# Kernel optimization log

Measured on AMD Instinct MI355X. Metric: run time of the kernel, lower is better.

The kernel has to match this reference:

```python
import jax, jax.numpy as jnp
import numpy as np

B, N, D, HID, S, NH = 2, 384, 768, 256, 64, 8


def layernorm(x, g, b, eps=1e-5):
    m = x.mean(-1, keepdims=True)
    v = ((x - m) ** 2).mean(-1, keepdims=True)
    return (x - m) * jax.lax.rsqrt(v + eps) * g + b


def setup_inputs() -> dict:
    key = jax.random.key(0)
    ks = jax.random.split(key, 32)
    r = lambda i, shp: jax.random.normal(ks[i], shp, dtype=jnp.float32) * 0.02
    inp = {
        'coordinates': jax.random.normal(ks[0], (B, N, 3), dtype=jnp.float32),
        'features': jax.random.normal(ks[1], (B, N, D), dtype=jnp.float32),
        'superpoint_labels': jax.random.randint(ks[2], (B, N), 0, S),
        # geometric_encoder: Linear(9,HID)-LN-ReLU-Linear(HID,D)-LN
        'ge_w1': r(3, (9, HID)), 'ge_b1': jnp.zeros((HID,)),
        'ge_g1': jnp.ones((HID,)), 'ge_be1': jnp.zeros((HID,)),
        'ge_w2': r(4, (HID, D)), 'ge_b2': jnp.zeros((D,)),
        'ge_g2': jnp.ones((D,)), 'ge_be2': jnp.zeros((D,)),
        # superpoint_aggregator: Linear(D,HID)-LN-ReLU-Linear(HID,D)-LN
        'ag_w1': r(5, (D, HID)), 'ag_b1': jnp.zeros((HID,)),
        'ag_g1': jnp.ones((HID,)), 'ag_be1': jnp.zeros((HID,)),
        'ag_w2': r(6, (HID, D)), 'ag_b2': jnp.zeros((D,)),
        'ag_g2': jnp.ones((D,)), 'ag_be2': jnp.zeros((D,)),
        # spatial_attention (MultiheadAttention, 8 heads)
        'wq': r(7, (D, D)), 'bq': jnp.zeros((D,)),
        'wk': r(8, (D, D)), 'bk': jnp.zeros((D,)),
        'wv': r(9, (D, D)), 'bv': jnp.zeros((D,)),
        'wo': r(10, (D, D)), 'bo': jnp.zeros((D,)),
    }
    return inp


def _forward(coordinates, features, superpoint_labels,
             ge_w1, ge_b1, ge_g1, ge_be1, ge_w2, ge_b2, ge_g2, ge_be2,
             ag_w1, ag_b1, ag_g1, ag_be1, ag_w2, ag_b2, ag_g2, ag_be2,
             wq, bq, wk, bk, wv, bv, wo, bo):
    # pairwise geometric relations: [B,N,N,9]
    rp = coordinates[:, :, None, :] - coordinates[:, None, :, :]
    dist = jnp.linalg.norm(rp, axis=-1, keepdims=True)
    rn = rp / jnp.maximum(dist, 1e-12)  # F.normalize semantics
    z = jnp.zeros_like(rn[..., 0])
    # torch loop writes channels (i*3+j-3): (0,1)->-2==3, (0,2)->-1==4, (1,2)->2; ch 0,1 stay zero
    ang = jnp.stack([z, z, rn[..., 1] * rn[..., 2],
                     rn[..., 0] * rn[..., 1], rn[..., 0] * rn[..., 2]], axis=-1)
    rel = jnp.concatenate([dist, rn, ang], axis=-1)
    h = jax.nn.relu(layernorm(rel @ ge_w1 + ge_b1, ge_g1, ge_be1))
    enc = layernorm(h @ ge_w2 + ge_b2, ge_g2, ge_be2)  # [B,N,N,D]
    geo_ctx = enc.mean(axis=2)  # [B,N,D]
    # per-superpoint scatter-mean (vectorized over all groups)
    oh = jax.nn.one_hot(superpoint_labels, S, dtype=features.dtype)  # [B,N,S]
    cnt = oh.sum(axis=1)  # [B,S]
    denom = jnp.maximum(cnt, 1.0)[..., None]
    mean_f = jnp.einsum('bns,bnd->bsd', oh, features) / denom
    mean_g = jnp.einsum('bns,bnd->bsd', oh, geo_ctx) / denom
    ah = jax.nn.relu(layernorm(mean_f @ ag_w1 + ag_b1, ag_g1, ag_be1))
    agg = layernorm(ah @ ag_w2 + ag_b2, ag_g2, ag_be2)
    combined = agg + mean_g  # [B,S,D]
    bidx = jnp.arange(B)[:, None]
    comb_g = combined[bidx, superpoint_labels]  # gather back [B,N,D]
    valid = (cnt[bidx, superpoint_labels] >= 2.0)[..., None]
    cw = 0.3  # consistency_weight
    enhanced = jnp.where(valid, (1.0 - cw) * features + cw * comb_g, features)
    # cross-attention: q=enhanced, k=v=geo_ctx
    dh = D // NH
    q = (enhanced @ wq + bq).reshape(B, N, NH, dh).transpose(0, 2, 1, 3)
    k = (geo_ctx @ wk + bk).reshape(B, N, NH, dh).transpose(0, 2, 1, 3)
    v = (geo_ctx @ wv + bv).reshape(B, N, NH, dh).transpose(0, 2, 1, 3)
    attn = jax.nn.softmax(jnp.einsum('bhqd,bhkd->bhqk', q, k) * (dh ** -0.5), axis=-1)
    o = jnp.einsum('bhqk,bhkd->bhqd', attn, v).transpose(0, 2, 1, 3).reshape(B, N, D)
    spatial = o @ wo + bo
    return enhanced + 0.5 * spatial


def reference(coordinates, features, superpoint_labels,
              ge_w1, ge_b1, ge_g1, ge_be1, ge_w2, ge_b2, ge_g2, ge_be2,
              ag_w1, ag_b1, ag_g1, ag_be1, ag_w2, ag_b2, ag_g2, ag_be2,
              wq, bq, wk, bk, wv, bv, wo, bo):
    return _forward(coordinates, features, superpoint_labels,
                    ge_w1, ge_b1, ge_g1, ge_be1, ge_w2, ge_b2, ge_g2, ge_be2,
                    ag_w1, ag_b1, ag_g1, ag_be1, ag_w2, ag_b2, ag_g2, ag_be2,
                    wq, bq, wk, bk, wv, bv, wo, bo)
```

## Files before the change

kernel.cpp:

```cpp
#include <hip/hip_runtime.h>
#include <hip/hip_bf16.h>
#include <stdint.h>
#include <stddef.h>

#define BB 2
#define NN 384
#define DD 768
#define HH 256
#define SS 64
#define NHH 8
#define DHH 96

typedef __attribute__((ext_vector_type(8))) short bf16x8;
typedef __attribute__((ext_vector_type(4))) float f32x4;

__device__ __forceinline__ float bits_f(unsigned short u){
  unsigned x = ((unsigned)u) << 16; float f; __builtin_memcpy(&f, &x, 4); return f;
}
__device__ __forceinline__ unsigned short f_bits(float a){
  unsigned x; __builtin_memcpy(&x, &a, 4);
  unsigned r = x + 0x7fffu + ((x >> 16) & 1u);
  return (unsigned short)(r >> 16);
}
__device__ __forceinline__ float lo_f(unsigned u){ unsigned x = u << 16; float f; __builtin_memcpy(&f,&x,4); return f; }
// ... 113 lines not shown
    f32x4 acc = (f32x4){0.f,0.f,0.f,0.f};
    for (int ks = 0; ks < 24; ++ks){
      bf16x8 af = *(const bf16x8*)&w2r[(size_t)(ti*16 + l16)*768 + ks*32 + quad*8];
      bf16x8 bf = *(const bf16x8*)&w2r[(size_t)(tj*16 + l16)*768 + ks*32 + quad*8];
      acc = __builtin_amdgcn_mfma_f32_16x16x32_bf16(af, bf, acc, 0,0,0);
    }
    #pragma unroll
    for (int r = 0; r < 4; ++r)
      Gm[(ti*16 + quad*4 + r)*256 + tj*16 + l16] = (short)f_bits(acc[r]);
  } else if (blk == 64){
    for (int c = tid; c < 768; c += 256) b2s[c] = b2[c];
    __syncthreads();
    float sa = 0.f, wa = 0.f;
    const uint4* wr = (const uint4*)(w2r + (size_t)tid*768);
    #pragma unroll 4
    for (int kk = 0; kk < 96; ++kk){
      uint4 ww = wr[kk];
      const float* bp = &b2s[kk*8];
      float x0=lo_f(ww.x), x1=hi_f(ww.x), x2=lo_f(ww.y), x3=hi_f(ww.y);
      float x4=lo_f(ww.z), x5=hi_f(ww.z), x6=lo_f(ww.w), x7=hi_f(ww.w);
      sa += (x0+x1)+(x2+x3)+(x4+x5)+(x6+x7);
      wa += bp[0]*x0 + bp[1]*x1 + bp[2]*x2 + bp[3]*x3
          + bp[4]*x4 + bp[5]*x5 + bp[6]*x6 + bp[7]*x7;
    }
    Gm[256*256 + tid] = (short)f_bits(sa);
    Gm[257*256 + tid] = (short)f_bits(wa);
    #pragma unroll
    for (int rr = 258; rr < 288; ++rr) Gm[rr*256 + tid] = 0;
    float pb = 0.f, pbb = 0.f;
    for (int c = tid; c < 768; c += 256){ float bb = b2s[c]; pb += bb; pbb += bb*bb; }
    for (int m = 32; m >= 1; m >>= 1){ pb += __shfl_xor(pb,m); pbb += __shfl_xor(pbb,m); }
    if ((tid & 63) == 0){ red[tid>>6] = pb; red[4+(tid>>6)] = pbb; }
    __syncthreads();
    if (tid == 0){ gscal[0] = red[0]+red[1]+red[2]+red[3]; gscal[1] = red[4]+red[5]+red[6]+red[7]; }
  } else {
    const unsigned short* w1u = (const unsigned short*)w1t;
    if (tid < 81){
      int i = tid / 9, j = tid % 9;
      float acc = 0.f;
      for (int c = 0; c < 256; ++c)
        acc += bits_f(w1u[c*32 + i]) * bits_f(w1u[c*32 + j]);
      g1s[18 + tid] = acc;
    } else if (tid < 90){
      int i = tid - 81;
      float sa = 0.f, sb = 0.f;
      for (int c = 0; c < 256; ++c){
        float x = bits_f(w1u[c*32 + i]);
        sa += x; sb += x * b1[c];
      }
      g1s[i] = sa; g1s[9 + i] = sb;
    } else if (tid == 90){
      float pb = 0.f, pbb = 0.f;
      for (int c = 0; c < 256; ++c){ float bb = b1[c]; pb += bb; pbb += bb*bb; }
      g1s[99] = pb; g1s[100] = pbb;
    }
  }
}

__global__ __launch_bounds__(256, 3) void k_geo(
    const float* __restrict__ coord, const short* __restrict__ w1t,
    const float* __restrict__ b1g, const float* __restrict__ g1g, const float* __restrict__ be1g,
    const short* __restrict__ Gm, const float* __restrict__ gscal,
    const float* __restrict__ g1s, float* __restrict__ gv)
{
  __shared__ short relbf[64*36];
  __shared__ short h_bf[64*256];
  __shared__ float rmean[64], rrstd[64];
  __shared__ float msum[64], wbsum[64], qsum[64];

  const int tid = threadIdx.x;
  const int pair = blockIdx.x % 768;
  const int jt   = blockIdx.x / 768;
  const int j0 = jt * 64;
  const int b = pair / NN;

  if (tid < 64){
    int j = j0 + tid;
    float cix = coord[pair*3+0], ciy = coord[pair*3+1], ciz = coord[pair*3+2];
    float dx = cix - coord[(b*NN+j)*3+0];
    float dy = ciy - coord[(b*NN+j)*3+1];
    float dz = ciz - coord[(b*NN+j)*3+2];
    float dist = sqrtf(dx*dx + dy*dy + dz*dz);
    float inv = 1.f / fmaxf(dist, 1e-12f);
    float x = dx*inv, y = dy*inv, z = dz*inv;
    float rv[9];
    rv[0]=dist; rv[1]=x; rv[2]=y; rv[3]=z; rv[4]=0.f; rv[5]=0.f;
    rv[6]=y*z; rv[7]=x*y; rv[8]=x*z;
    short* rr = &relbf[tid*36];
    float rbf[9];
    #pragma unroll
    for (int k=0;k<9;++k){
      unsigned short hb = f_bits(rv[k]);
      rr[k] = (short)hb; rbf[k] = bits_f(hb);
    }
    #pragma unroll
    for (int k=9;k<32;++k) rr[k]=0;
    float s = g1s[99], ssq = g1s[100];
    #pragma unroll
    for (int i=0;i<9;++i){
      s += rbf[i]*g1s[i];
      ssq += 2.f*rbf[i]*g1s[9+i];
      #pragma unroll
      for (int jj=0;jj<9;++jj) ssq += rbf[i]*rbf[jj]*g1s[18+i*9+jj];
    }
    float mean = s*(1.f/256.f);
    float var  = ssq*(1.f/256.f) - mean*mean;
    rmean[tid] = mean; rrstd[tid] = rsqrtf(var + 1e-5f);
  } else if (tid < 128){
    qsum[tid-64] = 0.f;
  }
  __syncthreads();

  const int wave = tid >> 6, lane = tid & 63, quad = lane >> 4, l16 = lane & 15;

  unsigned hreg[4][4][2];
  {
    bf16x8 af[4];
    #pragma unroll
    for (int rb=0;rb<4;++rb)
      af[rb] = *(const bf16x8*)&relbf[(rb*16 + l16)*36 + quad*8];
    f32x4 hacc[4][4];
    #pragma unroll
    for (int ci=0;ci<4;++ci){
      int cb = wave*4 + ci;
      bf16x8 bfw = *(const bf16x8*)&w1t[(cb*16 + l16)*32 + quad*8];
      #pragma unroll
      for (int rb=0;rb<4;++rb)
        hacc[ci][rb] = __builtin_amdgcn_mfma_f32_16x16x32_bf16(af[rb], bfw, (f32x4){0.f,0.f,0.f,0.f}, 0,0,0);
    }
    f32x4 rmv[4], rsv[4];
    #pragma unroll
    for (int rb=0;rb<4;++rb){
      rmv[rb] = *(const f32x4*)&rmean[rb*16 + quad*4];
      rsv[rb] = *(const f32x4*)&rrstd[rb*16 + quad*4];
    }
    #pragma unroll
    for (int ci=0;ci<4;++ci){
      int col = (wave*4+ci)*16 + l16;
      float b1c = b1g[col], g1c = g1g[col], be1c = be1g[col];
      int chb = col >> 3, lo = col & 7;
      #pragma unroll
      for (int rb=0;rb<4;++rb){
        float hn[4];
        #pragma unroll
        for (int r=0;r<4;++r)
          hn[r] = fmaxf((hacc[ci][rb][r] + b1c - rmv[rb][r]) * rsv[rb][r] * g1c + be1c, 0.f);
        unsigned p0 = cvt_pk_bf16(hn[0], hn[1]);
        unsigned p1 = cvt_pk_bf16(hn[2], hn[3]);
        hreg[ci][rb][0] = p0; hreg[ci][rb][1] = p1;
        int row0 = rb*16 + quad*4;
        h_bf[(row0+0)*256 + ((chb + row0+0)&31)*8 + lo] = (short)(p0 & 0xffff);
        h_bf[(row0+1)*256 + ((chb + row0+1)&31)*8 + lo] = (short)(p0 >> 16);
        h_bf[(row0+2)*256 + ((chb + row0+2)&31)*8 + lo] = (short)(p1 & 0xffff);
        h_bf[(row0+3)*256 + ((chb + row0+3)&31)*8 + lo] = (short)(p1 >> 16);
      }
    }
  }
  __syncthreads();

  {
    f32x4 acc[4][4];
    #pragma unroll
    for (int ci=0;ci<4;++ci)
      #pragma unroll
      for (int rb=0;rb<4;++rb) acc[ci][rb] = (f32x4){0.f,0.f,0.f,0.f};
    f32x4 eacc[4];
    #pragma unroll
    for (int rb=0;rb<4;++rb) eacc[rb] = (f32x4){0.f,0.f,0.f,0.f};
    for (int ks=0;ks<8;++ks){
      bf16x8 a4[4];
      #pragma unroll
      for (int rb=0;rb<4;++rb){
        int row = rb*16 + l16;
        a4[rb] = *(const bf16x8*)&h_bf[row*256 + (((ks*4 + quad) + row)&31)*8];
      }
      #pragma unroll
      for (int ci=0;ci<4;++ci){
        int n = (wave*4+ci)*16 + l16;
        bf16x8 bg = *(const bf16x8*)&Gm[n*256 + ks*32 + quad*8];
        #pragma unroll
        for (int rb=0;rb<4;++rb)
          acc[ci][rb] = __builtin_amdgcn_mfma_f32_16x16x32_bf16(a4[rb], bg, acc[ci][rb], 0,0,0);
      }
      if (wave == 0){
        bf16x8 bge = *(const bf16x8*)&Gm[(256 + l16)*256 + ks*32 + quad*8];
        #pragma unroll
        for (int rb=0;rb<4;++rb)
          eacc[rb] = __builtin_amdgcn_mfma_f32_16x16x32_bf16(a4[rb], bge, eacc[rb], 0,0,0);
      }
    }
    if (wave == 0 && l16 < 2){
      float* dst = (l16 == 0) ? msum : wbsum;
      #pragma unroll
      for (int rb=0;rb<4;++rb)
        #pragma unroll
        for (int r=0;r<4;++r) dst[rb*16 + quad*4 + r] = eacc[rb][r];
    }
    #pragma unroll
    for (int rb=0;rb<4;++rb){
      #pragma unroll
      for (int r=0;r<4;++r){
        int row = rb*16 + quad*4 + r;
        float qp = 0.f;
        #pragma unroll
        for (int ci=0;ci<4;++ci){
          unsigned p = hreg[ci][rb][r>>1];
          float hv = (r & 1) ? hi_f(p) : lo_f(p);
          qp += acc[ci][rb][r] * hv;
        }
        qp += __shfl_xor(qp,1);
        qp += __shfl_xor(qp,2);
        qp += __shfl_xor(qp,4);
        qp += __shfl_xor(qp,8);
        if (l16 == 0) atomicAdd(&qsum[row], qp);
      }
    }
  }
  __syncthreads();
  if (tid < 64){
    float Sb = gscal[0], Sbb = gscal[1];
    float m2 = (msum[tid] + Sb)*(1.f/768.f);
    float ssq = qsum[tid] + 2.f*wbsum[tid] + Sbb;
    float var = ssq*(1.f/768.f) - m2*m2;
    rmean[tid] = m2; rrstd[tid] = rsqrtf(var + 1e-5f);
  }
  __syncthreads();
  float* gp = gv + ((size_t)pair*6 + jt)*258;
  if (tid < 64){
    float rr = rrstd[tid], tt = rmean[tid]*rrstd[tid];
    for (int m = 32; m >= 1; m >>= 1){ rr += __shfl_xor(rr,m); tt += __shfl_xor(tt,m); }
    if (tid == 0){ gp[256] = rr; gp[257] = tt; }
  }
  {
    float vp[4] = {0.f, 0.f, 0.f, 0.f};
    #pragma unroll
    for (int rb=0;rb<4;++rb){
      #pragma unroll
      for (int r=0;r<4;++r){
        int row = rb*16 + quad*4 + r;
        float rs = rrstd[row];
        #pragma unroll
        for (int ci=0;ci<4;++ci){
          unsigned p = hreg[ci][rb][r>>1];
          float hv = (r & 1) ? hi_f(p) : lo_f(p);
          vp[ci] += rs * hv;
        }
      }
    }
    #pragma unroll
    for (int ci=0;ci<4;++ci){
      vp[ci] += __shfl_xor(vp[ci],16);
      vp[ci] += __shfl_xor(vp[ci],32);
    }
    if (quad == 0){
      #pragma unroll
      for (int ci=0;ci<4;++ci)
        gp[(wave*4+ci)*16 + l16] = vp[ci];
    }
  }
}

__global__ __launch_bounds__(256) void k_geofin(
    const float* __restrict__ gv, const short* __restrict__ w2r,
    const float* __restrict__ b2g, const float* __restrict__ g2g,
    const float* __restrict__ be2g, unsigned short* __restrict__ geo)
{
  __shared__ float V[256];
  __shared__ float RT[2];
  const int tid = threadIdx.x, pair = blockIdx.x;
  const float* gp = gv + (size_t)pair*6*258;
  V[tid] = gp[tid] + gp[258 + tid] + gp[2*258 + tid]
         + gp[3*258 + tid] + gp[4*258 + tid] + gp[5*258 + tid];
  if (tid < 2){
    float r = 0.f;
    #pragma unroll
    for (int t = 0; t < 6; ++t) r += gp[t*258 + 256 + tid];
    RT[tid] = r;
  }
  __syncthreads();
  const float R = RT[0], T = RT[1];
  const unsigned short* wr = (const unsigned short*)w2r;
  float a0 = 0.f, a1 = 0.f, a2 = 0.f;
  #pragma unroll 4
  for (int k = 0; k < 256; ++k){
    float vk = V[k];
    const unsigned short* row = wr + (size_t)k*768;
    a0 += vk * bits_f(row[tid]);
    a1 += vk * bits_f(row[tid+256]);
    a2 += vk * bits_f(row[tid+512]);
  }
  size_t base = (size_t)pair*DD;
  geo[base + tid]       = f_bits(g2g[tid]    *(a0 + b2g[tid]    *R - T)*(1.f/384.f) + be2g[tid]);
  geo[base + tid + 256] = f_bits(g2g[tid+256]*(a1 + b2g[tid+256]*R - T)*(1.f/384.f) + be2g[tid+256]);
  geo[base + tid + 512] = f_bits(g2g[tid+512]*(a2 + b2g[tid+512]*R - T)*(1.f/384.f) + be2g[tid+512]);
}

__global__ __launch_bounds__(256) void k_agg(
    const int* __restrict__ lab, const float* __restrict__ feat,
    const unsigned short* __restrict__ geo, float* __restrict__ cntw,
    const short* __restrict__ w1T, const float* __restrict__ b1g,
    const float* __restrict__ g1g, const float* __restrict__ be1g,
    const short* __restrict__ w2T, const float* __restrict__ b2g,
    const float* __restrict__ g2g, const float* __restrict__ be2g,
    float* __restrict__ comb)
{
  __shared__ int ls[NN];
  __shared__ float xr[DD];
  __shared__ float hr[HH];
  __shared__ float red[8];
  const int tid = threadIdx.x;
  const int bs = blockIdx.x, b = bs >> 6, s = bs & 63;
  for (int j = tid; j < NN; j += 256) ls[j] = lab[b*NN + j];
  __syncthreads();
  float f0 = 0.f, f1 = 0.f, f2 = 0.f, gg0 = 0.f, gg1 = 0.f, gg2 = 0.f;
  int cnt = 0;
  for (int j = 0; j < NN; ++j){
    if (ls[j] == s){
      ++cnt;
      size_t rb = (size_t)(b*NN + j)*DD;
      f0  += feat[rb + tid];
      f1  += feat[rb + tid + 256];
      f2  += feat[rb + tid + 512];
      gg0 += bits_f(geo[rb + tid]);
      gg1 += bits_f(geo[rb + tid + 256]);
      gg2 += bits_f(geo[rb + tid + 512]);
    }
  }
  const float inv = 1.f / fmaxf((float)cnt, 1.f);
  if (tid == 0) cntw[bs] = (float)cnt;
  xr[tid]       = f0*inv;
  xr[tid + 256] = f1*inv;
  xr[tid + 512] = f2*inv;
  float gmean[3] = { gg0*inv, gg1*inv, gg2*inv };
  __syncthreads();
  float a = b1g[tid];
  {
    const uint4* wr = (const uint4*)(w1T + (size_t)tid*768);
    #pragma unroll 4
    for (int kk = 0; kk < 96; ++kk){
      uint4 ww = wr[kk];
      const float* xp = &xr[kk*8];
      a += xp[0]*lo_f(ww.x) + xp[1]*hi_f(ww.x)
         + xp[2]*lo_f(ww.y) + xp[3]*hi_f(ww.y)
         + xp[4]*lo_f(ww.z) + xp[5]*hi_f(ww.z)
         + xp[6]*lo_f(ww.w) + xp[7]*hi_f(ww.w);
    }
  }
  float sum1 = a, q1 = a*a;
  for (int m = 32; m >= 1; m >>= 1){ sum1 += __shfl_xor(sum1,m); q1 += __shfl_xor(q1,m); }
  if ((tid & 63) == 0){ red[tid>>6] = sum1; red[4+(tid>>6)] = q1; }
  __syncthreads();
  sum1 = red[0]+red[1]+red[2]+red[3]; q1 = red[4]+red[5]+red[6]+red[7];
  float mean = sum1*(1.f/HH), var = q1*(1.f/HH) - mean*mean, rstd = rsqrtf(var + 1e-5f);
  float h = fmaxf((a-mean)*rstd*g1g[tid] + be1g[tid], 0.f);
  hr[tid] = h;
  __syncthreads();
  float y[3];
  #pragma unroll
  for (int u = 0; u < 3; ++u){
    int c = tid + 256*u;
    float t = b2g[c];
    const uint4* wr = (const uint4*)(w2T + (size_t)c*256);
    #pragma unroll 4
    for (int kk = 0; kk < 32; ++kk){
      uint4 ww = wr[kk];
      const float* hp = &hr[kk*8];
      t += hp[0]*lo_f(ww.x) + hp[1]*hi_f(ww.x)
         + hp[2]*lo_f(ww.y) + hp[3]*hi_f(ww.y)
         + hp[4]*lo_f(ww.z) + hp[5]*hi_f(ww.z)
         + hp[6]*lo_f(ww.w) + hp[7]*hi_f(ww.w);
    }
    y[u] = t;
  }
  float s2 = y[0]+y[1]+y[2], q2 = y[0]*y[0]+y[1]*y[1]+y[2]*y[2];
  for (int m = 32; m >= 1; m >>= 1){ s2 += __shfl_xor(s2,m); q2 += __shfl_xor(q2,m); }
  __syncthreads();
  if ((tid & 63) == 0){ red[tid>>6] = s2; red[4+(tid>>6)] = q2; }
  __syncthreads();
  s2 = red[0]+red[1]+red[2]+red[3]; q2 = red[4]+red[5]+red[6]+red[7];
  float mean2 = s2*(1.f/DD), rstd2 = rsqrtf(q2*(1.f/DD) - mean2*mean2 + 1e-5f);
  size_t base = (size_t)bs * DD;
  #pragma unroll
  for (int u = 0; u < 3; ++u){
    int c = tid + 256*u;
    comb[base + c] = (y[u]-mean2)*rstd2*g2g[c] + be2g[c] + gmean[u];
  }
}

__global__ void k_enhance(const float* __restrict__ feat, const int* __restrict__ lab,
                          const float* __restrict__ cntw, const float* __restrict__ comb,
                          float* __restrict__ enh, unsigned short* __restrict__ enhb)
{
  int idx = blockIdx.x * 256 + threadIdx.x;
  int c = idx % DD; int bn = idx / DD; int b = bn / NN;
  int l = lab[bn];
  float f = feat[idx];
  float cg = comb[(size_t)(b*SS + l)*DD + c];
  float cnt = cntw[b*SS + l];
  float e = (cnt >= 2.0f) ? (0.7f*f + 0.3f*cg) : f;
  enh[idx] = e;
  enhb[idx] = f_bits(e);
}

__global__ __launch_bounds__(256, 4) void k_qkv(
    const unsigned short* __restrict__ enhb, const unsigned short* __restrict__ geo,
    const short* __restrict__ wqT, const short* __restrict__ wkT, const short* __restrict__ wvT,
    const float* __restrict__ bq, const float* __restrict__ bk, const float* __restrict__ bv,
    unsigned short* __restrict__ qo, unsigned short* __restrict__ ko, unsigned short* __restrict__ vo)
{
  const int tid = threadIdx.x, blk = blockIdx.x;
  const int m = blk / 144, rem = blk % 144;
  const int rt = rem / 3, ct = rem % 3;
  const int wave = tid >> 6, lane = tid & 63, quad = lane >> 4, l16 = lane & 15;
  const short* WT = (m==0)?wqT:(m==1)?wkT:wvT;
  const float* Bv = (m==0)?bq:(m==1)?bk:bv;
  unsigned short* Y = (m==0)?qo:(m==1)?ko:vo;
  const short* X = (const short*)((m==0)? enhb : geo);
  const float oscale = (m==0)? 0.10206207261596577f : 1.0f;
  const int row0 = rt*16;
  const int col0 = ct*256 + wave*64;

  f32x4 acc[4];
  #pragma unroll
  for (int cb=0;cb<4;++cb) acc[cb] = (f32x4){0.f,0.f,0.f,0.f};
  for (int ks = 0; ks < 24; ++ks){
    bf16x8 af = *(const bf16x8*)&X[(size_t)(row0 + l16)*DD + ks*32 + quad*8];
    #pragma unroll
    for (int cb=0;cb<4;++cb){
      bf16x8 bw = *(const bf16x8*)&WT[(size_t)(col0 + cb*16 + l16)*DD + ks*32 + quad*8];
      acc[cb] = __builtin_amdgcn_mfma_f32_16x16x32_bf16(af, bw, acc[cb], 0,0,0);
    }
  }
  #pragma unroll
  for (int cb=0;cb<4;++cb){
    int col = col0 + cb*16 + l16;
    float bb = Bv[col];
    #pragma unroll
    for (int r=0;r<4;++r){
      int row = row0 + quad*4 + r;
      Y[(size_t)row*DD + col] = f_bits((acc[cb][r] + bb)*oscale);
    }
  }
}

__global__ __launch_bounds__(256) void k_attn_split(
    const unsigned short* __restrict__ qws, const unsigned short* __restrict__ kws,
    const unsigned short* __restrict__ vws, float* __restrict__ pws)
{
  __shared__ short kt[64*104];
  __shared__ short vt[64*104];
  __shared__ float st[32*66];
  __shared__ float lsum[32];
  const int tid = threadIdx.x;
  const int half = blockIdx.x / 192;
  const int inner = blockIdx.x % 192;
  const int b = inner / (NHH*12); int rem = inner % (NHH*12);
  const int h = rem / 12; const int qt = rem % 12; const int q0 = qt*32;
  const int sq = tid >> 3, jp = tid & 7;
  const int qp = tid >> 4, dp = tid & 15;
  unsigned qreg[48];
  {
    const unsigned* qr = (const unsigned*)(qws + (size_t)(b*NN + q0 + sq)*DD + h*DHH);
    #pragma unroll
    for (int d2 = 0; d2 < 48; ++d2) qreg[d2] = qr[d2];
  }
  if (tid < 32) lsum[tid] = 0.f;
  float Oacc[2][6];
  #pragma unroll
  for (int a = 0; a < 2; ++a)
    #pragma unroll
    for (int m = 0; m < 6; ++m) Oacc[a][m] = 0.f;

  for (int jt = half*3; jt < half*3 + 3; ++jt){
    const int j0 = jt * 64;
    __syncthreads();
    for (int x = tid; x < 64*48; x += 256){
      int jl = x / 48, du = x % 48;
      size_t rowoff = (size_t)(b*NN + j0 + jl)*DD + h*DHH;
      ((unsigned*)&kt[jl*104])[du] = ((const unsigned*)(kws + rowoff))[du];
      ((unsigned*)&vt[jl*104])[du] = ((const unsigned*)(vws + rowoff))[du];
    }
    __syncthreads();
    float lpart = 0.f;
    #pragma unroll
    for (int jj = 0; jj < 8; ++jj){
      int j = jp*8 + jj;
      const uint4* kr4 = (const uint4*)&kt[j*104];
      float s = 0.f;
      #pragma unroll
      for (int d4 = 0; d4 < 12; ++d4){
        uint4 kk = kr4[d4];
        unsigned q0r = qreg[4*d4], q1r = qreg[4*d4+1], q2r = qreg[4*d4+2], q3r = qreg[4*d4+3];
        s += lo_f(kk.x)*lo_f(q0r) + hi_f(kk.x)*hi_f(q0r);
        s += lo_f(kk.y)*lo_f(q1r) + hi_f(kk.y)*hi_f(q1r);
        s += lo_f(kk.z)*lo_f(q2r) + hi_f(kk.z)*hi_f(q2r);
        s += lo_f(kk.w)*lo_f(q3r) + hi_f(kk.w)*hi_f(q3r);
      }
      float p = __expf(s);
      st[sq*66 + j] = p;
      lpart += p;
    }
    lpart += __shfl_xor(lpart,1);
    lpart += __shfl_xor(lpart,2);
    lpart += __shfl_xor(lpart,4);
    if (jp == 0) lsum[sq] += lpart;
    __syncthreads();
    #pragma unroll 4
    for (int j = 0; j < 64; ++j){
      float p0 = st[(2*qp)*66 + j];
      float p1 = st[(2*qp+1)*66 + j];
      const unsigned* vr = (const unsigned*)&vt[j*104 + dp*6];
      #pragma unroll
      for (int m = 0; m < 3; ++m){
        unsigned vv = vr[m];
        float v0 = lo_f(vv), v1 = hi_f(vv);
        Oacc[0][2*m]   += p0*v0; Oacc[0][2*m+1] += p0*v1;
        Oacc[1][2*m]   += p1*v0; Oacc[1][2*m+1] += p1*v1;
      }
    }
  }
  __syncthreads();
  float* pb = pws + ((size_t)inner*2 + half)*3104;
  #pragma unroll
  for (int m = 0; m < 6; ++m){
    pb[(2*qp)*96 + dp*6 + m]   = Oacc[0][m];
    pb[(2*qp+1)*96 + dp*6 + m] = Oacc[1][m];
  }
  if (tid < 32) pb[3072 + tid] = lsum[tid];
}

__global__ __launch_bounds__(256) void k_attnfin(
    const float* __restrict__ pws, unsigned short* __restrict__ ows)
{
  __shared__ float ls[32];
  const int tid = threadIdx.x, inner = blockIdx.x;
  const int b = inner / (NHH*12); int rem = inner % (NHH*12);
  const int h = rem / 12; const int qt = rem % 12; const int q0 = qt*32;
  const float* p0 = pws + (size_t)inner*2*3104;
  const float* p1 = p0 + 3104;
  if (tid < 32) ls[tid] = 1.f / (p0[3072+tid] + p1[3072+tid]);
  __syncthreads();
  #pragma unroll
  for (int u = 0; u < 12; ++u){
    int e = tid + u*256;
    int q = e / 96, d = e % 96;
    float o = (p0[e] + p1[e]) * ls[q];
    ows[(size_t)(b*NN + q0 + q)*DD + h*DHH + d] = f_bits(o);
  }
}

__global__ __launch_bounds__(256) void k_attn_full(
    const unsigned short* __restrict__ qws, const unsigned short* __restrict__ kws,
    const unsigned short* __restrict__ vws, unsigned short* __restrict__ ows)
{
  __shared__ short kt[64*104];
  __shared__ short vt[64*104];
  __shared__ float st[32*66];
  __shared__ float lsum[32];
  const int tid = threadIdx.x;
  const int blk = blockIdx.x;
  const int b = blk / (NHH*12); int rem = blk % (NHH*12);
  const int h = rem / 12; const int qt = rem % 12; const int q0 = qt*32;
  const int sq = tid >> 3, jp = tid & 7;
  const int qp = tid >> 4, dp = tid & 15;
  unsigned qreg[48];
  {
    const unsigned* qr = (const unsigned*)(qws + (size_t)(b*NN + q0 + sq)*DD + h*DHH);
    #pragma unroll
    for (int d2 = 0; d2 < 48; ++d2) qreg[d2] = qr[d2];
  }
  if (tid < 32) lsum[tid] = 0.f;
  float Oacc[2][6];
  #pragma unroll
  for (int a = 0; a < 2; ++a)
    #pragma unroll
    for (int m = 0; m < 6; ++m) Oacc[a][m] = 0.f;
  for (int jt = 0; jt < 6; ++jt){
    const int j0 = jt * 64;
    __syncthreads();
    for (int x = tid; x < 64*48; x += 256){
      int jl = x / 48, du = x % 48;
      size_t rowoff = (size_t)(b*NN + j0 + jl)*DD + h*DHH;
      ((unsigned*)&kt[jl*104])[du] = ((const unsigned*)(kws + rowoff))[du];
      ((unsigned*)&vt[jl*104])[du] = ((const unsigned*)(vws + rowoff))[du];
    }
    __syncthreads();
    float lpart = 0.f;
    #pragma unroll
    for (int jj = 0; jj < 8; ++jj){
      int j = jp*8 + jj;
      const uint4* kr4 = (const uint4*)&kt[j*104];
      float s = 0.f;
      #pragma unroll
      for (int d4 = 0; d4 < 12; ++d4){
        uint4 kk = kr4[d4];
        unsigned q0r = qreg[4*d4], q1r = qreg[4*d4+1], q2r = qreg[4*d4+2], q3r = qreg[4*d4+3];
        s += lo_f(kk.x)*lo_f(q0r) + hi_f(kk.x)*hi_f(q0r);
        s += lo_f(kk.y)*lo_f(q1r) + hi_f(kk.y)*hi_f(q1r);
        s += lo_f(kk.z)*lo_f(q2r) + hi_f(kk.z)*hi_f(q2r);
        s += lo_f(kk.w)*lo_f(q3r) + hi_f(kk.w)*hi_f(q3r);
      }
      float p = __expf(s);
      st[sq*66 + j] = p;
      lpart += p;
    }
    lpart += __shfl_xor(lpart,1);
    lpart += __shfl_xor(lpart,2);
    lpart += __shfl_xor(lpart,4);
    if (jp == 0) lsum[sq] += lpart;
    __syncthreads();
    #pragma unroll 4
    for (int j = 0; j < 64; ++j){
      float p0 = st[(2*qp)*66 + j];
      float p1 = st[(2*qp+1)*66 + j];
      const unsigned* vr = (const unsigned*)&vt[j*104 + dp*6];
      #pragma unroll
      for (int m = 0; m < 3; ++m){
        unsigned vv = vr[m];
        float v0 = lo_f(vv), v1 = hi_f(vv);
        Oacc[0][2*m]   += p0*v0; Oacc[0][2*m+1] += p0*v1;
        Oacc[1][2*m]   += p1*v0; Oacc[1][2*m+1] += p1*v1;
      }
    }
  }
  __syncthreads();
  float l0 = 1.f / lsum[2*qp], l1 = 1.f / lsum[2*qp+1];
  size_t ob = (size_t)(b*NN + q0)*DD + h*DHH + dp*6;
  #pragma unroll
  for (int m = 0; m < 6; ++m){
    ows[ob + (size_t)(2*qp)*DD + m]   = f_bits(Oacc[0][m]*l0);
    ows[ob + (size_t)(2*qp+1)*DD + m] = f_bits(Oacc[1][m]*l1);
  }
}

__global__ __launch_bounds__(256, 4) void k_out(
    const unsigned short* __restrict__ ows, const float* __restrict__ enh,
    const short* __restrict__ woT, const float* __restrict__ bo, float* __restrict__ out)
{
  const int tid = threadIdx.x, blk = blockIdx.x;
  const int rt = blk / 3, ct = blk % 3;
  const int wave = tid >> 6, lane = tid & 63, quad = lane >> 4, l16 = lane & 15;
  const int row0 = rt*16;
  const int col0 = ct*256 + wave*64;
  f32x4 acc[4];
  #pragma unroll
  for (int cb=0;cb<4;++cb) acc[cb] = (f32x4){0.f,0.f,0.f,0.f};
  for (int ks = 0; ks < 24; ++ks){
    bf16x8 af = *(const bf16x8*)&((const short*)ows)[(size_t)(row0 + l16)*DD + ks*32 + quad*8];
    #pragma unroll
    for (int cb=0;cb<4;++cb){
      bf16x8 bw = *(const bf16x8*)&woT[(size_t)(col0 + cb*16 + l16)*DD + ks*32 + quad*8];
      acc[cb] = __builtin_amdgcn_mfma_f32_16x16x32_bf16(af, bw, acc[cb], 0,0,0);
    }
  }
  #pragma unroll
  for (int cb=0;cb<4;++cb){
    int col = col0 + cb*16 + l16;
    float bb = bo[col];
    #pragma unroll
    for (int r=0;r<4;++r){
      size_t idx = (size_t)(row0 + quad*4 + r)*DD + col;
      out[idx] = enh[idx] + 0.5f*(acc[cb][r] + bb);
    }
  }
}

extern "C" void kernel_launch(void* const* d_in, const int* in_sizes, int n_in,
                              void* d_out, int out_size, void* d_ws, size_t ws_size,
                              hipStream_t stream) {
  const float* coord = (const float*)d_in[0];
  const float* feat  = (const float*)d_in[1];
  const int*   lab   = (const int*)d_in[2];
  const float* ge_w1 = (const float*)d_in[3];
  const float* ge_b1 = (const float*)d_in[4];
  const float* ge_g1 = (const float*)d_in[5];
  const float* ge_be1= (const float*)d_in[6];
  const float* ge_w2 = (const float*)d_in[7];
  const float* ge_b2 = (const float*)d_in[8];
  const float* ge_g2 = (const float*)d_in[9];
  const float* ge_be2= (const float*)d_in[10];
  const float* ag_w1 = (const float*)d_in[11];
  const float* ag_b1 = (const float*)d_in[12];
  const float* ag_g1 = (const float*)d_in[13];
  const float* ag_be1= (const float*)d_in[14];
  const float* ag_w2 = (const float*)d_in[15];
  const float* ag_b2 = (const float*)d_in[16];
  const float* ag_g2 = (const float*)d_in[17];
  const float* ag_be2= (const float*)d_in[18];
  const float* wq = (const float*)d_in[19];
  const float* bq = (const float*)d_in[20];
  const float* wk = (const float*)d_in[21];
  const float* bk = (const float*)d_in[22];
  const float* wv = (const float*)d_in[23];
  const float* bv = (const float*)d_in[24];
  const float* wo = (const float*)d_in[25];
  const float* bo = (const float*)d_in[26];

  char* w = (char*)d_ws;
  unsigned short* geo_bf = (unsigned short*)(w);
  float*          enh_f  = (float*)(w + 1179648);
  unsigned short* enh_bf = (unsigned short*)(w + 3538944);
  unsigned short* qw_bf  = (unsigned short*)(w + 4718592);
  unsigned short* kw_bf  = (unsigned short*)(w + 5898240);
  unsigned short* vw_bf  = (unsigned short*)(w + 7077888);
  float*          gv     = (float*)(w + 4718592);
  float*          cntw   = (float*)(w + 9842688);
  float*          comb   = (float*)(w + 9843200);
  short*          w2T    = (short*)(w + 10236416);
  short*          w2r    = (short*)(w + 10629632);
  short*          w1t    = (short*)(w + 11022848);
  short*          Gm     = (short*)(w + 11039232);
  float*          g1s    = (float*)(w + 11186688);
  float*          gscal  = (float*)(w + 11187200);
  short*          wqT    = (short*)(w + 11187456);
  short*          wkT    = (short*)(w + 12367104);
  short*          wvT    = (short*)(w + 13546752);
  short*          woT    = (short*)(w + 14726400);
  short*          agw1T  = (short*)(w + 15906048);
  short*          agw2T  = (short*)(w + 16299264);
  float*          pws    = (float*)(w + 16692480);
  unsigned short* ow_bf  = geo_bf;
  const bool split_attn = (ws_size >= 21460224);

  hipLaunchKernelGGL(k_prep,    dim3(1520),  dim3(256), 0, stream,
                     ge_w2, ge_w1, wq, wk, wv, wo, ag_w1, ag_w2,
                     w2T, w2r, wqT, wkT, wvT, woT, w1t, agw1T, agw2T);
  hipLaunchKernelGGL(k_gprep,   dim3(66),    dim3(256), 0, stream,
                     w2r, ge_b2, w1t, ge_b1, Gm, gscal, g1s);
  hipLaunchKernelGGL(k_geo,     dim3(4608),  dim3(256), 0, stream,
                     coord, w1t, ge_b1, ge_g1, ge_be1, Gm, gscal, g1s, gv);
  hipLaunchKernelGGL(k_geofin,  dim3(768),   dim3(256), 0, stream,
                     gv, w2r, ge_b2, ge_g2, ge_be2, geo_bf);
  hipLaunchKernelGGL(k_agg,     dim3(128),   dim3(256), 0, stream,
                     lab, feat, geo_bf, cntw, agw1T, ag_b1, ag_g1, ag_be1,
                     agw2T, ag_b2, ag_g2, ag_be2, comb);
  hipLaunchKernelGGL(k_enhance, dim3(2304),  dim3(256), 0, stream,
                     feat, lab, cntw, comb, enh_f, enh_bf);
  hipLaunchKernelGGL(k_qkv,     dim3(432),   dim3(256), 0, stream,
                     enh_bf, geo_bf, wqT, wkT, wvT, bq, bk, bv, qw_bf, kw_bf, vw_bf);
  if (split_attn){
    hipLaunchKernelGGL(k_attn_split, dim3(384), dim3(256), 0, stream,
                       qw_bf, kw_bf, vw_bf, pws);
    hipLaunchKernelGGL(k_attnfin,    dim3(192), dim3(256), 0, stream,
                       pws, ow_bf);
  } else {
    hipLaunchKernelGGL(k_attn_full,  dim3(192), dim3(256), 0, stream,
                       qw_bf, kw_bf, vw_bf, ow_bf);
  }
  hipLaunchKernelGGL(k_out,     dim3(144),   dim3(256), 0, stream,
                     ow_bf, enh_f, woT, bo, (float*)d_out);
}
```

Measured before the change: 426.6 us.

## Fuse enhance into QKV/out GEMMs and attention finalize into output projection

Removes the standalone enhance kernel by recomputing the consistency blend on the fly inside the Q projection's A-operand load and the output epilogue. It also drops the split-attention finalize kernel: the output projection reads both fp32 partials and the row sums directly, normalising and converting them to bf16 as it loads. This saves two launches and the enh/ows intermediate round-trips. In exchange it reads fp32 data, twice the bytes of the bf16 tiles it replaces, inside the GEMM inner loops, and repeats the blend for each column tile.

```diff
diff --git a/kernel.cpp b/kernel.cpp
--- a/kernel.cpp
+++ b/kernel.cpp
@@ -524,23 +524,10 @@
   }
 }
 
-__global__ void k_enhance(const float* __restrict__ feat, const int* __restrict__ lab,
-                          const float* __restrict__ cntw, const float* __restrict__ comb,
-                          float* __restrict__ enh, unsigned short* __restrict__ enhb)
-{
-  int idx = blockIdx.x * 256 + threadIdx.x;
-  int c = idx % DD; int bn = idx / DD; int b = bn / NN;
-  int l = lab[bn];
-  float f = feat[idx];
-  float cg = comb[(size_t)(b*SS + l)*DD + c];
-  float cnt = cntw[b*SS + l];
-  float e = (cnt >= 2.0f) ? (0.7f*f + 0.3f*cg) : f;
-  enh[idx] = e;
-  enhb[idx] = f_bits(e);
-}
-
 __global__ __launch_bounds__(256, 4) void k_qkv(
-    const unsigned short* __restrict__ enhb, const unsigned short* __restrict__ geo,
+    const float* __restrict__ feat, const int* __restrict__ lab,
+    const float* __restrict__ cntw, const float* __restrict__ comb,
+    const unsigned short* __restrict__ geo,
     const short* __restrict__ wqT, const short* __restrict__ wkT, const short* __restrict__ wvT,
     const float* __restrict__ bq, const float* __restrict__ bk, const float* __restrict__ bv,
     unsigned short* __restrict__ qo, unsigned short* __restrict__ ko, unsigned short* __restrict__ vo)
@@ -552,16 +539,48 @@
   const short* WT = (m==0)?wqT:(m==1)?wkT:wvT;
   const float* Bv = (m==0)?bq:(m==1)?bk:bv;
   unsigned short* Y = (m==0)?qo:(m==1)?ko:vo;
-  const short* X = (const short*)((m==0)? enhb : geo);
+  const short* X = (const short*)geo;
   const float oscale = (m==0)? 0.10206207261596577f : 1.0f;
   const int row0 = rt*16;
   const int col0 = ct*256 + wave*64;
 
+  const int arow = row0 + l16;
+  const float* fr = nullptr; const float* cr = nullptr; bool valid = false;
+  if (m == 0){
+    int ab = arow / NN; int l = lab[arow];
+    valid = (cntw[ab*SS + l] >= 2.0f);
+    fr = feat + (size_t)arow*DD;
+    cr = comb + (size_t)(ab*SS + l)*DD;
+  }
+
   f32x4 acc[4];
   #pragma unroll
   for (int cb=0;cb<4;++cb) acc[cb] = (f32x4){0.f,0.f,0.f,0.f};
   for (int ks = 0; ks < 24; ++ks){
-    bf16x8 af = *(const bf16x8*)&X[(size_t)(row0 + l16)*DD + ks*32 + quad*8];
+    bf16x8 af;
+    if (m == 0){
+      int c0 = ks*32 + quad*8;
+      float4 f0 = *(const float4*)&fr[c0];
+      float4 f1 = *(const float4*)&fr[c0+4];
+      float4 g0 = *(const float4*)&cr[c0];
+      float4 g1 = *(const float4*)&cr[c0+4];
+      float e0 = valid ? (0.7f*f0.x + 0.3f*g0.x) : f0.x;
+      float e1 = valid ? (0.7f*f0.y + 0.3f*g0.y) : f0.y;
+      float e2 = valid ? (0.7f*f0.z + 0.3f*g0.z) : f0.z;
+      float e3 = valid ? (0.7f*f0.w + 0.3f*g0.w) : f0.w;
+      float e4 = valid ? (0.7f*f1.x + 0.3f*g1.x) : f1.x;
+      float e5 = valid ? (0.7f*f1.y + 0.3f*g1.y) : f1.y;
+      float e6 = valid ? (0.7f*f1.z + 0.3f*g1.z) : f1.z;
+      float e7 = valid ? (0.7f*f1.w + 0.3f*g1.w) : f1.w;
+      union { unsigned u[4]; bf16x8 v; } au;
+      au.u[0] = cvt_pk_bf16(e0, e1);
+      au.u[1] = cvt_pk_bf16(e2, e3);
+      au.u[2] = cvt_pk_bf16(e4, e5);
+      au.u[3] = cvt_pk_bf16(e6, e7);
+      af = au.v;
+    } else {
+      af = *(const bf16x8*)&X[(size_t)arow*DD + ks*32 + quad*8];
+    }
     #pragma unroll
     for (int cb=0;cb<4;++cb){
       bf16x8 bw = *(const bf16x8*)&WT[(size_t)(col0 + cb*16 + l16)*DD + ks*32 + quad*8];
@@ -666,26 +685,6 @@
   if (tid < 32) pb[3072 + tid] = lsum[tid];
 }
 
-__global__ __launch_bounds__(256) void k_attnfin(
-    const float* __restrict__ pws, unsigned short* __restrict__ ows)
-{
-  __shared__ float ls[32];
-  const int tid = threadIdx.x, inner = blockIdx.x;
-  const int b = inner / (NHH*12); int rem = inner % (NHH*12);
-  const int h = rem / 12; const int qt = rem % 12; const int q0 = qt*32;
-  const float* p0 = pws + (size_t)inner*2*3104;
-  const float* p1 = p0 + 3104;
-  if (tid < 32) ls[tid] = 1.f / (p0[3072+tid] + p1[3072+tid]);
-  __syncthreads();
-  #pragma unroll
-  for (int u = 0; u < 12; ++u){
-    int e = tid + u*256;
-    int q = e / 96, d = e % 96;
-    float o = (p0[e] + p1[e]) * ls[q];
-    ows[(size_t)(b*NN + q0 + q)*DD + h*DHH + d] = f_bits(o);
-  }
-}
-
 __global__ __launch_bounds__(256) void k_attn_full(
     const unsigned short* __restrict__ qws, const unsigned short* __restrict__ kws,
     const unsigned short* __restrict__ vws, unsigned short* __restrict__ ows)
@@ -770,8 +769,81 @@
   }
 }
 
-__global__ __launch_bounds__(256, 4) void k_out(
-    const unsigned short* __restrict__ ows, const float* __restrict__ enh,
+__global__ __launch_bounds__(256, 4) void k_out_pws(
+    const float* __restrict__ pws, const float* __restrict__ feat,
+    const int* __restrict__ lab, const float* __restrict__ cntw,
+    const float* __restrict__ comb,
+    const short* __restrict__ woT, const float* __restrict__ bo, float* __restrict__ out)
+{
+  const int tid = threadIdx.x, blk = blockIdx.x;
+  const int rt = blk / 3, ct = blk % 3;
+  const int wave = tid >> 6, lane = tid & 63, quad = lane >> 4, l16 = lane & 15;
+  const int row0 = rt*16;
+  const int col0 = ct*256 + wave*64;
+
+  const int arow = row0 + l16;
+  const int ab = arow / NN, an = arow % NN;
+  const int aqt = an >> 5, aql = an & 31;
+  float lsv[8];
+  #pragma unroll
+  for (int h = 0; h < 8; ++h){
+    const float* q0p = pws + ((size_t)(ab*96 + h*12 + aqt)*2)*3104 + 3072 + aql;
+    lsv[h] = 1.f/(q0p[0] + q0p[3104]);
+  }
+
+  f32x4 acc[4];
+  #pragma unroll
+  for (int cb=0;cb<4;++cb) acc[cb] = (f32x4){0.f,0.f,0.f,0.f};
+  for (int ks = 0; ks < 24; ++ks){
+    int c0 = ks*32 + quad*8;
+    int h = c0 / 96, d0 = c0 % 96;
+    const float* pp0 = pws + ((size_t)(ab*96 + h*12 + aqt)*2)*3104 + (size_t)aql*96 + d0;
+    const float* pp1 = pp0 + 3104;
+    float4 x0 = *(const float4*)&pp0[0];
+    float4 x1 = *(const float4*)&pp0[4];
+    float4 y0 = *(const float4*)&pp1[0];
+    float4 y1 = *(const float4*)&pp1[4];
+    float ls = lsv[h];
+    union { unsigned u[4]; bf16x8 v; } au;
+    au.u[0] = cvt_pk_bf16((x0.x+y0.x)*ls, (x0.y+y0.y)*ls);
+    au.u[1] = cvt_pk_bf16((x0.z+y0.z)*ls, (x0.w+y0.w)*ls);
+    au.u[2] = cvt_pk_bf16((x1.x+y1.x)*ls, (x1.y+y1.y)*ls);
+    au.u[3] = cvt_pk_bf16((x1.z+y1.z)*ls, (x1.w+y1.w)*ls);
+    bf16x8 af = au.v;
+    #pragma unroll
+    for (int cb=0;cb<4;++cb){
+      bf16x8 bw = *(const bf16x8*)&woT[(size_t)(col0 + cb*16 + l16)*DD + ks*32 + quad*8];
+      acc[cb] = __builtin_amdgcn_mfma_f32_16x16x32_bf16(af, bw, acc[cb], 0,0,0);
+    }
+  }
+  const float* frv[4]; const float* crv[4]; bool vav[4];
+  #pragma unroll
+  for (int r=0;r<4;++r){
+    int row = row0 + quad*4 + r;
+    int bb_ = row / NN; int l = lab[row];
+    vav[r] = (cntw[bb_*SS + l] >= 2.0f);
+    frv[r] = feat + (size_t)row*DD;
+    crv[r] = comb + (size_t)(bb_*SS + l)*DD;
+  }
+  #pragma unroll
+  for (int cb=0;cb<4;++cb){
+    int col = col0 + cb*16 + l16;
+    float bb = bo[col];
+    #pragma unroll
+    for (int r=0;r<4;++r){
+      int row = row0 + quad*4 + r;
+      float f = frv[r][col];
+      float cg = crv[r][col];
+      float e = vav[r] ? (0.7f*f + 0.3f*cg) : f;
+      out[(size_t)row*DD + col] = e + 0.5f*(acc[cb][r] + bb);
+    }
+  }
+}
+
+__global__ __launch_bounds__(256, 4) void k_out_bf(
+    const unsigned short* __restrict__ ows, const float* __restrict__ feat,
+    const int* __restrict__ lab, const float* __restrict__ cntw,
+    const float* __restrict__ comb,
     const short* __restrict__ woT, const float* __restrict__ bo, float* __restrict__ out)
 {
   const int tid = threadIdx.x, blk = blockIdx.x;
@@ -790,14 +862,26 @@
       acc[cb] = __builtin_amdgcn_mfma_f32_16x16x32_bf16(af, bw, acc[cb], 0,0,0);
     }
   }
+  const float* frv[4]; const float* crv[4]; bool vav[4];
+  #pragma unroll
+  for (int r=0;r<4;++r){
+    int row = row0 + quad*4 + r;
+    int bb_ = row / NN; int l = lab[row];
+    vav[r] = (cntw[bb_*SS + l] >= 2.0f);
+    frv[r] = feat + (size_t)row*DD;
+    crv[r] = comb + (size_t)(bb_*SS + l)*DD;
+  }
   #pragma unroll
   for (int cb=0;cb<4;++cb){
     int col = col0 + cb*16 + l16;
     float bb = bo[col];
     #pragma unroll
     for (int r=0;r<4;++r){
-      size_t idx = (size_t)(row0 + quad*4 + r)*DD + col;
-      out[idx] = enh[idx] + 0.5f*(acc[cb][r] + bb);
+      int row = row0 + quad*4 + r;
+      float f = frv[r][col];
+      float cg = crv[r][col];
+      float e = vav[r] ? (0.7f*f + 0.3f*cg) : f;
+      out[(size_t)row*DD + col] = e + 0.5f*(acc[cb][r] + bb);
     }
   }
 }
@@ -835,8 +919,6 @@
 
   char* w = (char*)d_ws;
   unsigned short* geo_bf = (unsigned short*)(w);
-  float*          enh_f  = (float*)(w + 1179648);
-  unsigned short* enh_bf = (unsigned short*)(w + 3538944);
   unsigned short* qw_bf  = (unsigned short*)(w + 4718592);
   unsigned short* kw_bf  = (unsigned short*)(w + 5898240);
   unsigned short* vw_bf  = (unsigned short*)(w + 7077888);
@@ -871,19 +953,18 @@
   hipLaunchKernelGGL(k_agg,     dim3(128),   dim3(256), 0, stream,
                      lab, feat, geo_bf, cntw, agw1T, ag_b1, ag_g1, ag_be1,
                      agw2T, ag_b2, ag_g2, ag_be2, comb);
-  hipLaunchKernelGGL(k_enhance, dim3(2304),  dim3(256), 0, stream,
-                     feat, lab, cntw, comb, enh_f, enh_bf);
   hipLaunchKernelGGL(k_qkv,     dim3(432),   dim3(256), 0, stream,
-                     enh_bf, geo_bf, wqT, wkT, wvT, bq, bk, bv, qw_bf, kw_bf, vw_bf);
+                     feat, lab, cntw, comb, geo_bf, wqT, wkT, wvT,
+                     bq, bk, bv, qw_bf, kw_bf, vw_bf);
   if (split_attn){
     hipLaunchKernelGGL(k_attn_split, dim3(384), dim3(256), 0, stream,
                        qw_bf, kw_bf, vw_bf, pws);
-    hipLaunchKernelGGL(k_attnfin,    dim3(192), dim3(256), 0, stream,
-                       pws, ow_bf);
+    hipLaunchKernelGGL(k_out_pws,    dim3(144), dim3(256), 0, stream,
+                       pws, feat, lab, cntw, comb, woT, bo, (float*)d_out);
   } else {
     hipLaunchKernelGGL(k_attn_full,  dim3(192), dim3(256), 0, stream,
                        qw_bf, kw_bf, vw_bf, ow_bf);
-  }
-  hipLaunchKernelGGL(k_out,     dim3(144),   dim3(256), 0, stream,
-                     ow_bf, enh_f, woT, bo, (float*)d_out);
-}
+    hipLaunchKernelGGL(k_out_bf,     dim3(144), dim3(256), 0, stream,
+                       ow_bf, feat, lab, cntw, comb, woT, bo, (float*)d_out);
+  }
+}
```

Result: slower. 444.0 us (+4.1%).

## Batch 16 superpoints per block in aggregator and use bf16 MFMA for MLP

Applied to the files above, without the earlier changes.

The superpoint aggregator now handles 16 superpoints per block (8 blocks instead of 128). Each wave accumulates feature and geometry sums for 4 superpoints in one pass over the labels. Both MLP layers run as 16-row bf16 MFMA GEMMs with LayerNorm statistics reduced through shared-memory atomics, so weights are read once per 16 superpoints instead of once per superpoint. The trade-offs are that only 8 blocks fill a large GPU, the first-layer activations are rounded to bf16, and the geometry means take an extra round trip through global memory.

```diff
diff --git a/kernel.cpp b/kernel.cpp
--- a/kernel.cpp
+++ b/kernel.cpp
@@ -439,88 +439,200 @@
     const float* __restrict__ g1g, const float* __restrict__ be1g,
     const short* __restrict__ w2T, const float* __restrict__ b2g,
     const float* __restrict__ g2g, const float* __restrict__ be2g,
-    float* __restrict__ comb)
+    float* __restrict__ gmean, float* __restrict__ comb)
 {
   __shared__ int ls[NN];
-  __shared__ float xr[DD];
-  __shared__ float hr[HH];
-  __shared__ float red[8];
+  __shared__ short xA[16*776];
+  __shared__ short hA[16*264];
+  __shared__ float rsum[16], rsq[16], rmean[16], rrstd[16];
+
   const int tid = threadIdx.x;
-  const int bs = blockIdx.x, b = bs >> 6, s = bs & 63;
+  const int wave = tid >> 6, lane = tid & 63, quad = lane >> 4, l16 = lane & 15;
+  const int bs0 = blockIdx.x * 16;
+  const int b = bs0 >> 6;
+  const int swbase = (bs0 & 63) + wave*4;
+
   for (int j = tid; j < NN; j += 256) ls[j] = lab[b*NN + j];
-  __syncthreads();
-  float f0 = 0.f, f1 = 0.f, f2 = 0.f, gg0 = 0.f, gg1 = 0.f, gg2 = 0.f;
-  int cnt = 0;
+  if (tid < 16){ rsum[tid] = 0.f; rsq[tid] = 0.f; }
+  __syncthreads();
+
+  float r0a[12], r1a[12], r2a[12], r3a[12];
+  float g0a[12], g1a[12], g2a[12], g3a[12];
+  #pragma unroll
+  for (int e=0;e<12;++e){
+    r0a[e]=0.f; r1a[e]=0.f; r2a[e]=0.f; r3a[e]=0.f;
+    g0a[e]=0.f; g1a[e]=0.f; g2a[e]=0.f; g3a[e]=0.f;
+  }
+  int c0=0, c1=0, c2=0, c3=0;
   for (int j = 0; j < NN; ++j){
-    if (ls[j] == s){
-      ++cnt;
-      size_t rb = (size_t)(b*NN + j)*DD;
-      f0  += feat[rb + tid];
-      f1  += feat[rb + tid + 256];
-      f2  += feat[rb + tid + 512];
-      gg0 += bits_f(geo[rb + tid]);
-      gg1 += bits_f(geo[rb + tid + 256]);
-      gg2 += bits_f(geo[rb + tid + 512]);
-    }
-  }
-  const float inv = 1.f / fmaxf((float)cnt, 1.f);
-  if (tid == 0) cntw[bs] = (float)cnt;
-  xr[tid]       = f0*inv;
-  xr[tid + 256] = f1*inv;
-  xr[tid + 512] = f2*inv;
-  float gmean[3] = { gg0*inv, gg1*inv, gg2*inv };
-  __syncthreads();
-  float a = b1g[tid];
+    int ridx = ls[j] - swbase;
+    if ((unsigned)ridx < 4u){
+      size_t rb = (size_t)(b*NN + j)*DD + lane;
+      float fv[12], gw[12];
+      #pragma unroll
+      for (int e=0;e<12;++e){ fv[e] = feat[rb + e*64]; gw[e] = bits_f(geo[rb + e*64]); }
+      if (ridx == 0){
+        ++c0;
+        #pragma unroll
+        for (int e=0;e<12;++e){ r0a[e]+=fv[e]; g0a[e]+=gw[e]; }
+      } else if (ridx == 1){
+        ++c1;
+        #pragma unroll
+        for (int e=0;e<12;++e){ r1a[e]+=fv[e]; g1a[e]+=gw[e]; }
+      } else if (ridx == 2){
+        ++c2;
+        #pragma unroll
+        for (int e=0;e<12;++e){ r2a[e]+=fv[e]; g2a[e]+=gw[e]; }
+      } else {
+        ++c3;
+        #pragma unroll
+        for (int e=0;e<12;++e){ r3a[e]+=fv[e]; g3a[e]+=gw[e]; }
+      }
+    }
+  }
   {
-    const uint4* wr = (const uint4*)(w1T + (size_t)tid*768);
-    #pragma unroll 4
-    for (int kk = 0; kk < 96; ++kk){
-      uint4 ww = wr[kk];
-      const float* xp = &xr[kk*8];
-      a += xp[0]*lo_f(ww.x) + xp[1]*hi_f(ww.x)
-         + xp[2]*lo_f(ww.y) + xp[3]*hi_f(ww.y)
-         + xp[4]*lo_f(ww.z) + xp[5]*hi_f(ww.z)
-         + xp[6]*lo_f(ww.w) + xp[7]*hi_f(ww.w);
-    }
-  }
-  float sum1 = a, q1 = a*a;
-  for (int m = 32; m >= 1; m >>= 1){ sum1 += __shfl_xor(sum1,m); q1 += __shfl_xor(q1,m); }
-  if ((tid & 63) == 0){ red[tid>>6] = sum1; red[4+(tid>>6)] = q1; }
-  __syncthreads();
-  sum1 = red[0]+red[1]+red[2]+red[3]; q1 = red[4]+red[5]+red[6]+red[7];
-  float mean = sum1*(1.f/HH), var = q1*(1.f/HH) - mean*mean, rstd = rsqrtf(var + 1e-5f);
-  float h = fmaxf((a-mean)*rstd*g1g[tid] + be1g[tid], 0.f);
-  hr[tid] = h;
-  __syncthreads();
-  float y[3];
-  #pragma unroll
-  for (int u = 0; u < 3; ++u){
-    int c = tid + 256*u;
-    float t = b2g[c];
-    const uint4* wr = (const uint4*)(w2T + (size_t)c*256);
-    #pragma unroll 4
-    for (int kk = 0; kk < 32; ++kk){
-      uint4 ww = wr[kk];
-      const float* hp = &hr[kk*8];
-      t += hp[0]*lo_f(ww.x) + hp[1]*hi_f(ww.x)
-         + hp[2]*lo_f(ww.y) + hp[3]*hi_f(ww.y)
-         + hp[4]*lo_f(ww.z) + hp[5]*hi_f(ww.z)
-         + hp[6]*lo_f(ww.w) + hp[7]*hi_f(ww.w);
-    }
-    y[u] = t;
-  }
-  float s2 = y[0]+y[1]+y[2], q2 = y[0]*y[0]+y[1]*y[1]+y[2]*y[2];
-  for (int m = 32; m >= 1; m >>= 1){ s2 += __shfl_xor(s2,m); q2 += __shfl_xor(q2,m); }
-  __syncthreads();
-  if ((tid & 63) == 0){ red[tid>>6] = s2; red[4+(tid>>6)] = q2; }
-  __syncthreads();
-  s2 = red[0]+red[1]+red[2]+red[3]; q2 = red[4]+red[5]+red[6]+red[7];
-  float mean2 = s2*(1.f/DD), rstd2 = rsqrtf(q2*(1.f/DD) - mean2*mean2 + 1e-5f);
-  size_t base = (size_t)bs * DD;
-  #pragma unroll
-  for (int u = 0; u < 3; ++u){
-    int c = tid + 256*u;
-    comb[base + c] = (y[u]-mean2)*rstd2*g2g[c] + be2g[c] + gmean[u];
+    const int row = wave*4;
+    float inv;
+    inv = 1.f/fmaxf((float)c0,1.f);
+    #pragma unroll
+    for (int e=0;e<12;++e){
+      int col = lane + e*64;
+      xA[(row+0)*776 + col] = (short)f_bits(r0a[e]*inv);
+      gmean[(size_t)(bs0+row+0)*DD + col] = g0a[e]*inv;
+    }
+    if (lane == 0) cntw[bs0+row+0] = (float)c0;
+    inv = 1.f/fmaxf((float)c1,1.f);
+    #pragma unroll
+    for (int e=0;e<12;++e){
+      int col = lane + e*64;
+      xA[(row+1)*776 + col] = (short)f_bits(r1a[e]*inv);
+      gmean[(size_t)(bs0+row+1)*DD + col] = g1a[e]*inv;
+    }
+    if (lane == 0) cntw[bs0+row+1] = (float)c1;
+    inv = 1.f/fmaxf((float)c2,1.f);
+    #pragma unroll
+    for (int e=0;e<12;++e){
+      int col = lane + e*64;
+      xA[(row+2)*776 + col] = (short)f_bits(r2a[e]*inv);
+      gmean[(size_t)(bs0+row+2)*DD + col] = g2a[e]*inv;
+    }
+    if (lane == 0) cntw[bs0+row+2] = (float)c2;
+    inv = 1.f/fmaxf((float)c3,1.f);
+    #pragma unroll
+    for (int e=0;e<12;++e){
+      int col = lane + e*64;
+      xA[(row+3)*776 + col] = (short)f_bits(r3a[e]*inv);
+      gmean[(size_t)(bs0+row+3)*DD + col] = g3a[e]*inv;
+    }
+    if (lane == 0) cntw[bs0+row+3] = (float)c3;
+  }
+  __threadfence_block();
+  __syncthreads();
+
+  f32x4 acc[4];
+  #pragma unroll
+  for (int cb=0;cb<4;++cb) acc[cb] = (f32x4){0.f,0.f,0.f,0.f};
+  for (int ks = 0; ks < 24; ++ks){
+    bf16x8 af = *(const bf16x8*)&xA[l16*776 + ks*32 + quad*8];
+    #pragma unroll
+    for (int cb=0;cb<4;++cb){
+      bf16x8 bw = *(const bf16x8*)&w1T[(size_t)(wave*64 + cb*16 + l16)*768 + ks*32 + quad*8];
+      acc[cb] = __builtin_amdgcn_mfma_f32_16x16x32_bf16(af, bw, acc[cb], 0,0,0);
+    }
+  }
+  {
+    float ps[4] = {0.f,0.f,0.f,0.f}, pq[4] = {0.f,0.f,0.f,0.f};
+    #pragma unroll
+    for (int cb=0;cb<4;++cb){
+      int col = wave*64 + cb*16 + l16;
+      float b1c = b1g[col];
+      #pragma unroll
+      for (int r=0;r<4;++r){
+        float v = acc[cb][r] + b1c;
+        acc[cb][r] = v;
+        ps[r] += v; pq[r] += v*v;
+      }
+    }
+    #pragma unroll
+    for (int r=0;r<4;++r){
+      ps[r] += __shfl_xor(ps[r],1); pq[r] += __shfl_xor(pq[r],1);
+      ps[r] += __shfl_xor(ps[r],2); pq[r] += __shfl_xor(pq[r],2);
+      ps[r] += __shfl_xor(ps[r],4); pq[r] += __shfl_xor(pq[r],4);
+      ps[r] += __shfl_xor(ps[r],8); pq[r] += __shfl_xor(pq[r],8);
+      if (l16 == 0){ atomicAdd(&rsum[quad*4+r], ps[r]); atomicAdd(&rsq[quad*4+r], pq[r]); }
+    }
+  }
+  __syncthreads();
+  if (tid < 16){
+    float mean = rsum[tid]*(1.f/HH);
+    float var  = rsq[tid]*(1.f/HH) - mean*mean;
+    rmean[tid] = mean; rrstd[tid] = rsqrtf(var + 1e-5f);
+    rsum[tid] = 0.f; rsq[tid] = 0.f;
+  }
+  __syncthreads();
+  #pragma unroll
+  for (int cb=0;cb<4;++cb){
+    int col = wave*64 + cb*16 + l16;
+    float g1c = g1g[col], be1c = be1g[col];
+    #pragma unroll
+    for (int r=0;r<4;++r){
+      int row = quad*4 + r;
+      float h = fmaxf((acc[cb][r]-rmean[row])*rrstd[row]*g1c + be1c, 0.f);
+      hA[row*264 + col] = (short)f_bits(h);
+    }
+  }
+  __syncthreads();
+
+  f32x4 acc2[12];
+  #pragma unroll
+  for (int cb=0;cb<12;++cb) acc2[cb] = (f32x4){0.f,0.f,0.f,0.f};
+  for (int ks = 0; ks < 8; ++ks){
+    bf16x8 af = *(const bf16x8*)&hA[l16*264 + ks*32 + quad*8];
+    #pragma unroll
+    for (int cb=0;cb<12;++cb){
+      bf16x8 bw = *(const bf16x8*)&w2T[(size_t)(wave*192 + cb*16 + l16)*256 + ks*32 + quad*8];
+      acc2[cb] = __builtin_amdgcn_mfma_f32_16x16x32_bf16(af, bw, acc2[cb], 0,0,0);
+    }
+  }
+  {
+    float ps[4] = {0.f,0.f,0.f,0.f}, pq[4] = {0.f,0.f,0.f,0.f};
+    #pragma unroll
+    for (int cb=0;cb<12;++cb){
+      int col = wave*192 + cb*16 + l16;
+      float b2c = b2g[col];
+      #pragma unroll
+      for (int r=0;r<4;++r){
+        float v = acc2[cb][r] + b2c;
+        acc2[cb][r] = v;
+        ps[r] += v; pq[r] += v*v;
+      }
+    }
+    #pragma unroll
+    for (int r=0;r<4;++r){
+      ps[r] += __shfl_xor(ps[r],1); pq[r] += __shfl_xor(pq[r],1);
+      ps[r] += __shfl_xor(ps[r],2); pq[r] += __shfl_xor(pq[r],2);
+      ps[r] += __shfl_xor(ps[r],4); pq[r] += __shfl_xor(pq[r],4);
+      ps[r] += __shfl_xor(ps[r],8); pq[r] += __shfl_xor(pq[r],8);
+      if (l16 == 0){ atomicAdd(&rsum[quad*4+r], ps[r]); atomicAdd(&rsq[quad*4+r], pq[r]); }
+    }
+  }
+  __syncthreads();
+  if (tid < 16){
+    float mean = rsum[tid]*(1.f/DD);
+    float var  = rsq[tid]*(1.f/DD) - mean*mean;
+    rmean[tid] = mean; rrstd[tid] = rsqrtf(var + 1e-5f);
+  }
+  __syncthreads();
+  #pragma unroll
+  for (int cb=0;cb<12;++cb){
+    int col = wave*192 + cb*16 + l16;
+    float g2c = g2g[col], be2c = be2g[col];
+    #pragma unroll
+    for (int r=0;r<4;++r){
+      int row = quad*4 + r;
+      size_t idx = (size_t)(bs0+row)*DD + col;
+      comb[idx] = (acc2[cb][r]-rmean[row])*rrstd[row]*g2c + be2c + gmean[idx];
+    }
   }
 }
 
@@ -841,6 +953,7 @@
   unsigned short* kw_bf  = (unsigned short*)(w + 5898240);
   unsigned short* vw_bf  = (unsigned short*)(w + 7077888);
   float*          gv     = (float*)(w + 4718592);
+  float*          gmean  = (float*)(w + 8257536);
   float*          cntw   = (float*)(w + 9842688);
   float*          comb   = (float*)(w + 9843200);
   short*          w2T    = (short*)(w + 10236416);
@@ -868,9 +981,9 @@
                      coord, w1t, ge_b1, ge_g1, ge_be1, Gm, gscal, g1s, gv);
   hipLaunchKernelGGL(k_geofin,  dim3(768),   dim3(256), 0, stream,
                      gv, w2r, ge_b2, ge_g2, ge_be2, geo_bf);
-  hipLaunchKernelGGL(k_agg,     dim3(128),   dim3(256), 0, stream,
+  hipLaunchKernelGGL(k_agg,     dim3(8),     dim3(256), 0, stream,
                      lab, feat, geo_bf, cntw, agw1T, ag_b1, ag_g1, ag_be1,
-                     agw2T, ag_b2, ag_g2, ag_be2, comb);
+                     agw2T, ag_b2, ag_g2, ag_be2, gmean, comb);
   hipLaunchKernelGGL(k_enhance, dim3(2304),  dim3(256), 0, stream,
                      feat, lab, cntw, comb, enh_f, enh_bf);
   hipLaunchKernelGGL(k_qkv,     dim3(432),   dim3(256), 0, stream,
```

Measured after the change: 450.1 us. 1.05x slower.
